# Performance work log

Hardware: AMD Instinct MI355X
Metric: run time of the kernel (lower is better)

Reference implementation:

```python
import jax, jax.numpy as jnp
import numpy as np

E = 8      # num_experts
K = 2      # active_experts
D = 1024   # embed_size
H = 4 * D  # ffn hidden


def setup_inputs() -> dict:
    key = jax.random.key(0)
    ks = jax.random.split(key, 7)
    s_in = 1.0 / np.sqrt(D)
    s_h = 1.0 / np.sqrt(H)
    return {
        "x":  jax.random.normal(ks[0], (4, 2048, D), dtype=jnp.float32),
        "Wr": jax.random.uniform(ks[1], (D, E), jnp.float32, -s_in, s_in),
        "br": jax.random.uniform(ks[2], (E,), jnp.float32, -s_in, s_in),
        "W1": jax.random.uniform(ks[3], (E, D, H), jnp.float32, -s_in, s_in),
        "b1": jax.random.uniform(ks[4], (E, H), jnp.float32, -s_in, s_in),
        "W2": jax.random.uniform(ks[5], (E, H, D), jnp.float32, -s_h, s_h),
        "b2": jax.random.uniform(ks[6], (E, D), jnp.float32, -s_h, s_h),
    }


def reference(x, Wr, br, W1, b1, W2, b2):
    # Router: softmax over experts, top-k values, renormalize.
    logits = jnp.einsum("bsd,de->bse", x, Wr) + br            # [B,S,E]
    probs = jax.nn.softmax(logits, axis=-1)
    topk_vals, _ = jax.lax.top_k(probs, K)                     # [B,S,K]
    gates = topk_vals / topk_vals.sum(axis=-1, keepdims=True)  # [B,S,K]

    # Original bug (reproduced faithfully): the mask-multiply-sum is identity,
    # and slot index i selects experts[i], so only experts 0..K-1 run on ALL tokens.
    h = jax.nn.relu(jnp.einsum("bsd,kdh->bskh", x, W1[:K]) + b1[:K])  # [B,S,K,H]
    y = jnp.einsum("bskh,khd->bskd", h, W2[:K]) + b2[:K]               # [B,S,K,D]
    return jnp.einsum("bskd,bsk->bsd", y, gates)                       # [B,S,D]
```

## Files before the change

kernel.cpp:

```cpp
#include <hip/hip_runtime.h>
#include <hip/hip_bf16.h>

#define T_TOK 8192
#define DDIM  1024
#define HDIM  4096
#define KCAT  8192
#define NE    8

typedef __attribute__((ext_vector_type(8))) __bf16 bf16x8;
typedef __attribute__((ext_vector_type(4))) float  f32x4;

__device__ __forceinline__ unsigned short f2bf(float f) {
  union { float f; unsigned u; } v; v.f = f;
  unsigned r = v.u + 0x7fffu + ((v.u >> 16) & 1u);
  return (unsigned short)(r >> 16);
}

__device__ __forceinline__ void gl_lds16(const unsigned short* g, char* l) {
  __builtin_amdgcn_global_load_lds(
      (__attribute__((address_space(1))) const void*)g,
      (__attribute__((address_space(3))) void*)l,
      16, 0, 0);
}

__global__ __launch_bounds__(256) void k_router(
    const float* __restrict__ x, const float* __restrict__ Wr,
    const float* __restrict__ br, unsigned short* __restrict__ xb,
    float* __restrict__ gates)
{
  const int lane = threadIdx.x & 63;
  const int wv   = threadIdx.x >> 6;
  const int t    = blockIdx.x * 4 + wv;
  const float* xr = x + (size_t)t * DDIM;
  unsigned short* xo = xb + (size_t)t * DDIM;

  float acc[NE];
#pragma unroll
  for (int e = 0; e < NE; ++e) acc[e] = 0.f;

#pragma unroll
  for (int i = 0; i < 4; ++i) {
    float4 v = *(const float4*)(xr + i * 256 + lane * 4);
    ushort4 o;
    o.x = f2bf(v.x); o.y = f2bf(v.y); o.z = f2bf(v.z); o.w = f2bf(v.w);
    *(ushort4*)(xo + i * 256 + lane * 4) = o;
    float vs[4] = {v.x, v.y, v.z, v.w};
#pragma unroll
    for (int j = 0; j < 4; ++j) {
      const float4* wr = (const float4*)(Wr + (size_t)(i * 256 + lane * 4 + j) * NE);
      float4 w0 = wr[0], w1 = wr[1];
      acc[0] += vs[j] * w0.x; acc[1] += vs[j] * w0.y;
      acc[2] += vs[j] * w0.z; acc[3] += vs[j] * w0.w;
      acc[4] += vs[j] * w1.x; acc[5] += vs[j] * w1.y;
      acc[6] += vs[j] * w1.z; acc[7] += vs[j] * w1.w;
    }
  }
#pragma unroll
  for (int e = 0; e < NE; ++e) {
#pragma unroll
    for (int s = 32; s > 0; s >>= 1) acc[e] += __shfl_xor(acc[e], s, 64);
  }
  if (lane == 0) {
    float lg[NE];
#pragma unroll
    for (int e = 0; e < NE; ++e) lg[e] = acc[e] + br[e];
    int a1 = 0; float m1 = lg[0];
#pragma unroll
    for (int e = 1; e < NE; ++e) if (lg[e] > m1) { m1 = lg[e]; a1 = e; }
    float m2 = -3.4e38f;
#pragma unroll
    for (int e = 0; e < NE; ++e) if (e != a1 && lg[e] > m2) m2 = lg[e];
    float g0 = 1.f / (1.f + expf(m2 - m1));
    gates[t * 2 + 0] = g0;
    gates[t * 2 + 1] = 1.f - g0;
  }
}

__global__ __launch_bounds__(256) void k_transpose(
    const float* __restrict__ in, unsigned short* __restrict__ out,
    int R, int C, int S, size_t inz, size_t outz)
{
  __shared__ float tile[32][33];
  in  += (size_t)blockIdx.z * inz;
  out += (size_t)blockIdx.z * outz;
  const int c0 = blockIdx.x * 32, r0 = blockIdx.y * 32;
  const int tx = threadIdx.x & 31, ty = threadIdx.x >> 5;
#pragma unroll
  for (int i = 0; i < 32; i += 8)
    tile[ty + i][tx] = in[(size_t)(r0 + ty + i) * C + (c0 + tx)];
  __syncthreads();
#pragma unroll
  for (int i = 0; i < 32; i += 8)
    out[(size_t)(c0 + ty + i) * S + (r0 + tx)] = f2bf(tile[tx][ty + i]);
}

template<int NT, int MODE>
__global__ __launch_bounds__(512, 2) void k_gemm8(
    const unsigned short* __restrict__ A,
    const unsigned short* __restrict__ B,
    unsigned short* __restrict__ Hout,
    float* __restrict__ P0, float* __restrict__ P1,
    const float* __restrict__ bias,
    const float* __restrict__ gates,
    int KA, int KB)
{
  constexpr int NIT = NT / 2;
  __shared__ __align__(16) char lds[2 * 4 * 16384];

  const int tid = threadIdx.x;
  const int l = tid & 63, g = (l >> 4), l15 = l & 15;
  const int w = tid >> 6;
  const int wm = w >> 2, wn = w & 3;

  int bmIdx, bnIdx, bzIdx;
  {
    int lin = ((blockIdx.z * gridDim.y) + blockIdx.y) * gridDim.x + blockIdx.x;
    int xcd = lin & 7, slot = (lin >> 3) & 31;
    if (MODE == 0) {
      int r = lin >> 8;
      bmIdx = r * 8 + (slot >> 2);
      bnIdx = xcd * 4 + (slot & 3);
      bzIdx = 0;
    } else {
      bzIdx = xcd & 1;
      bmIdx = (xcd >> 1) * 8 + (slot >> 2);
      bnIdx = slot & 3;
    }
  }
  const int bn = bnIdx * 256;
  const int bm = bmIdx * 256;
  const int koff = bzIdx * (NT * 64);

  const int srow = tid >> 2;
  const int sc = (tid & 3) ^ ((srow >> 1) & 3);
  const unsigned short* As = A + (size_t)(bm + srow) * KA + koff + sc * 8;
  const unsigned short* Bs = B + (size_t)(bn + srow) * KB + koff + sc * 8;

  auto stage = [&](int T, int reg) {
    const unsigned short* src = ((reg >> 1) ? Bs : As) + T * 64 + (reg & 1) * 32;
    size_t rstride = (size_t)128 * ((reg >> 1) ? KB : KA);
    char* dst = lds + (((T & 1) * 4 + reg) << 14) + tid * 16;
    gl_lds16(src, dst);
    gl_lds16(src + rstride, dst + 8192);
  };

  int aoff[2][4], boff[4];
#pragma unroll
  for (int mh = 0; mh < 2; ++mh)
#pragma unroll
    for (int mi = 0; mi < 4; ++mi) {
      int r = wm * 128 + mh * 64 + mi * 16 + l15;
      aoff[mh][mi] = r * 64 + ((g ^ ((r >> 1) & 3)) * 16);
    }
#pragma unroll
  for (int nj = 0; nj < 4; ++nj) {
    int r = wn * 64 + nj * 16 + l15;
    boff[nj] = r * 64 + ((g ^ ((r >> 1) & 3)) * 16);
  }

  f32x4 acc[8][4];
#pragma unroll
  for (int i = 0; i < 8; ++i)
#pragma unroll
    for (int j = 0; j < 4; ++j) acc[i][j] = (f32x4){0.f, 0.f, 0.f, 0.f};

  stage(0, 2); stage(0, 0); stage(0, 3); stage(0, 1);
  stage(1, 2); stage(1, 0); stage(1, 3);
  asm volatile("s_waitcnt vmcnt(6)" ::: "memory");
  __builtin_amdgcn_s_barrier();

#define MFMA16(AI, A0, A1, A2, A3)                                                     \
    acc[(AI)+0][0] = __builtin_amdgcn_mfma_f32_16x16x32_bf16(A0, vb0, acc[(AI)+0][0], 0,0,0); \
    acc[(AI)+0][1] = __builtin_amdgcn_mfma_f32_16x16x32_bf16(A0, vb1, acc[(AI)+0][1], 0,0,0); \
    acc[(AI)+0][2] = __builtin_amdgcn_mfma_f32_16x16x32_bf16(A0, vb2, acc[(AI)+0][2], 0,0,0); \
    acc[(AI)+0][3] = __builtin_amdgcn_mfma_f32_16x16x32_bf16(A0, vb3, acc[(AI)+0][3], 0,0,0); \
    acc[(AI)+1][0] = __builtin_amdgcn_mfma_f32_16x16x32_bf16(A1, vb0, acc[(AI)+1][0], 0,0,0); \
    acc[(AI)+1][1] = __builtin_amdgcn_mfma_f32_16x16x32_bf16(A1, vb1, acc[(AI)+1][1], 0,0,0); \
    acc[(AI)+1][2] = __builtin_amdgcn_mfma_f32_16x16x32_bf16(A1, vb2, acc[(AI)+1][2], 0,0,0); \
    acc[(AI)+1][3] = __builtin_amdgcn_mfma_f32_16x16x32_bf16(A1, vb3, acc[(AI)+1][3], 0,0,0); \
    acc[(AI)+2][0] = __builtin_amdgcn_mfma_f32_16x16x32_bf16(A2, vb0, acc[(AI)+2][0], 0,0,0); \
    acc[(AI)+2][1] = __builtin_amdgcn_mfma_f32_16x16x32_bf16(A2, vb1, acc[(AI)+2][1], 0,0,0); \
    acc[(AI)+2][2] = __builtin_amdgcn_mfma_f32_16x16x32_bf16(A2, vb2, acc[(AI)+2][2], 0,0,0); \
    acc[(AI)+2][3] = __builtin_amdgcn_mfma_f32_16x16x32_bf16(A2, vb3, acc[(AI)+2][3], 0,0,0); \
    acc[(AI)+3][0] = __builtin_amdgcn_mfma_f32_16x16x32_bf16(A3, vb0, acc[(AI)+3][0], 0,0,0); \
    acc[(AI)+3][1] = __builtin_amdgcn_mfma_f32_16x16x32_bf16(A3, vb1, acc[(AI)+3][1], 0,0,0); \
    acc[(AI)+3][2] = __builtin_amdgcn_mfma_f32_16x16x32_bf16(A3, vb2, acc[(AI)+3][2], 0,0,0); \
    acc[(AI)+3][3] = __builtin_amdgcn_mfma_f32_16x16x32_bf16(A3, vb3, acc[(AI)+3][3], 0,0,0);

#define MPH(BUF, KH, VM, STG1, STG2) do {                                      \
    const char* Ar_ = lds + (((BUF) * 4 + (KH)) << 14);                        \
    const char* Br_ = lds + (((BUF) * 4 + 2 + (KH)) << 14);                    \
    bf16x8 vb0 = *(const bf16x8*)(Br_ + boff[0]);                              \
    bf16x8 vb1 = *(const bf16x8*)(Br_ + boff[1]);                              \
    bf16x8 vb2 = *(const bf16x8*)(Br_ + boff[2]);                              \
    bf16x8 vb3 = *(const bf16x8*)(Br_ + boff[3]);                              \
    bf16x8 vc0 = *(const bf16x8*)(Ar_ + aoff[0][0]);                           \
    bf16x8 vc1 = *(const bf16x8*)(Ar_ + aoff[0][1]);                           \
    bf16x8 vc2 = *(const bf16x8*)(Ar_ + aoff[0][2]);                           \
    bf16x8 vc3 = *(const bf16x8*)(Ar_ + aoff[0][3]);                           \
    bf16x8 vn0 = *(const bf16x8*)(Ar_ + aoff[1][0]);                           \
    bf16x8 vn1 = *(const bf16x8*)(Ar_ + aoff[1][1]);                           \
    bf16x8 vn2 = *(const bf16x8*)(Ar_ + aoff[1][2]);                           \
    bf16x8 vn3 = *(const bf16x8*)(Ar_ + aoff[1][3]);                           \
    asm volatile("" ::: "memory");          \
    STG1; STG2;                                                                \
    if ((VM) == 6) asm volatile("s_waitcnt vmcnt(6)" ::: "memory");            \
    else if ((VM) == 0) asm volatile("s_waitcnt vmcnt(0)" ::: "memory");       \
    __builtin_amdgcn_s_barrier();                                              \
    __builtin_amdgcn_s_setprio(1);                                             \
    MFMA16(0, vc0, vc1, vc2, vc3)                                              \
    MFMA16(4, vn0, vn1, vn2, vn3)                                              \
    __builtin_amdgcn_s_setprio(0);                                             \
    __builtin_amdgcn_s_barrier();                                              \
  } while (0)

  for (int t = 0; t < NIT - 1; ++t) {
    MPH(0, 0, -1, stage(2 * t + 1, 1), stage(2 * t + 2, 2));
    MPH(0, 1,  6, stage(2 * t + 2, 0), stage(2 * t + 2, 3));
    MPH(1, 0, -1, stage(2 * t + 2, 1), stage(2 * t + 3, 2));
    MPH(1, 1,  6, stage(2 * t + 3, 0), stage(2 * t + 3, 3));
  }
  MPH(0, 0, -1, stage(NT - 1, 1), ;);
  MPH(0, 1,  0, ;, ;);
  MPH(1, 0, -1, ;, ;);
  MPH(1, 1, -1, ;, ;);
#undef MPH
#undef MFMA16

  if constexpr (MODE == 0) {
    const int ge = bn >> 12;
    float bcol[4];
#pragma unroll
    for (int nj = 0; nj < 4; ++nj) bcol[nj] = bias[bn + wn * 64 + nj * 16 + l15];
#pragma unroll
    for (int mi = 0; mi < 8; ++mi) {
#pragma unroll
      for (int rr = 0; rr < 4; ++rr) {
        int row = bm + wm * 128 + mi * 16 + g * 4 + rr;
        float gate = gates[row * 2 + ge];
        size_t rb = (size_t)row * KCAT + bn + wn * 64 + l15;
#pragma unroll
        for (int nj = 0; nj < 4; ++nj) {
          float v = acc[mi][nj][rr] + bcol[nj];
          Hout[rb + nj * 16] = f2bf(fmaxf(v, 0.f) * gate);
        }
      }
    }
  } else {
    float* P = bzIdx ? P1 : P0;
#pragma unroll
    for (int mi = 0; mi < 8; ++mi) {
#pragma unroll
      for (int rr = 0; rr < 4; ++rr) {
        int row = bm + wm * 128 + mi * 16 + g * 4 + rr;
        size_t rb = (size_t)row * DDIM + bn + wn * 64 + l15;
#pragma unroll
        for (int nj = 0; nj < 4; ++nj) P[rb + nj * 16] = acc[mi][nj][rr];
      }
    }
  }
}

__global__ __launch_bounds__(256) void k_combine(
    const float* __restrict__ P1, const float* __restrict__ b2,
    const float* __restrict__ gates, float* __restrict__ O)
{
  size_t i = ((size_t)blockIdx.x * 256 + threadIdx.x) * 4;
  int row = (int)(i >> 10), d = (int)(i & 1023);
  float g0 = gates[row * 2], g1 = gates[row * 2 + 1];
  float4 p0 = *(const float4*)(O + i);
  float4 p1 = *(const float4*)(P1 + i);
  float4 ba = *(const float4*)(b2 + d);
  float4 bb = *(const float4*)(b2 + DDIM + d);
  float4 r;
  r.x = p0.x + p1.x + g0 * ba.x + g1 * bb.x;
  r.y = p0.y + p1.y + g0 * ba.y + g1 * bb.y;
  r.z = p0.z + p1.z + g0 * ba.z + g1 * bb.z;
  r.w = p0.w + p1.w + g0 * ba.w + g1 * bb.w;
  *(float4*)(O + i) = r;
}

extern "C" void kernel_launch(void* const* d_in, const int* in_sizes, int n_in,
                              void* d_out, int out_size, void* d_ws, size_t ws_size,
                              hipStream_t stream) {
  const float* x  = (const float*)d_in[0];
  const float* Wr = (const float*)d_in[1];
  const float* br = (const float*)d_in[2];
  const float* W1 = (const float*)d_in[3];
  const float* b1 = (const float*)d_in[4];
  const float* W2 = (const float*)d_in[5];
  const float* b2 = (const float*)d_in[6];

  char* ws = (char*)d_ws;
  unsigned short* xb    = (unsigned short*)(ws);
  unsigned short* W1T   = (unsigned short*)(ws + (16u << 20));
  unsigned short* W2T   = (unsigned short*)(ws + (32u << 20));
  float*          gates = (float*)(ws + (48u << 20));
  unsigned short* hbuf  = (unsigned short*)(ws + (49u << 20));
  float*          P1    = (float*)(ws);

  k_router<<<dim3(T_TOK / 4), dim3(256), 0, stream>>>(x, Wr, br, xb, gates);

  k_transpose<<<dim3(HDIM / 32, DDIM / 32, 2), dim3(256), 0, stream>>>(
      W1, W1T, DDIM, HDIM, DDIM, (size_t)DDIM * HDIM, (size_t)HDIM * DDIM);
  k_transpose<<<dim3(DDIM / 32, HDIM / 32, 2), dim3(256), 0, stream>>>(
      W2, W2T, HDIM, DDIM, KCAT, (size_t)HDIM * DDIM, (size_t)HDIM);

  k_gemm8<16, 0><<<dim3(KCAT / 256, T_TOK / 256, 1), dim3(512), 0, stream>>>(
      xb, W1T, hbuf, nullptr, nullptr, b1, gates, DDIM, DDIM);

  k_gemm8<64, 1><<<dim3(DDIM / 256, T_TOK / 256, 2), dim3(512), 0, stream>>>(
      hbuf, W2T, nullptr, (float*)d_out, P1, nullptr, nullptr, KCAT, KCAT);

  k_combine<<<dim3(T_TOK * DDIM / 4 / 256), dim3(256), 0, stream>>>(
      P1, b2, gates, (float*)d_out);
}
```

Baseline: 325.7 us.

## Restructure GEMM pipeline into four-stage ring of 32-wide K tiles

Replaces the two-buffer scheme with 64-wide K tiles split into halves by a four-buffer ring of 32-wide K tiles, each holding A and B. Loads run three stages ahead, with vmcnt waits adjusted to 8/4/0. The aim is deeper prefetch so global-to-LDS latency hides behind MFMA work. LDS size stays at 128KB, and the tail handling and wait counts must be exactly right for correctness.

```diff
diff --git a/kernel.cpp b/kernel.cpp
--- a/kernel.cpp
+++ b/kernel.cpp
@@ -95,7 +95,7 @@
 }
 
 template<int NT, int MODE>
-__global__ __launch_bounds__(512, 2) void k_gemm8(
+__global__ __launch_bounds__(512, 2) void k_gemm4(
     const unsigned short* __restrict__ A,
     const unsigned short* __restrict__ B,
     unsigned short* __restrict__ Hout,
@@ -104,8 +104,7 @@
     const float* __restrict__ gates,
     int KA, int KB)
 {
-  constexpr int NIT = NT / 2;
-  __shared__ __align__(16) char lds[2 * 4 * 16384];
+  __shared__ __align__(16) char lds[4 * 32768];
 
   const int tid = threadIdx.x;
   const int l = tid & 63, g = (l >> 4), l15 = l & 15;
@@ -129,7 +128,7 @@
   }
   const int bn = bnIdx * 256;
   const int bm = bmIdx * 256;
-  const int koff = bzIdx * (NT * 64);
+  const int koff = bzIdx * (NT * 32);
 
   const int srow = tid >> 2;
   const int sc = (tid & 3) ^ ((srow >> 1) & 3);
@@ -137,9 +136,9 @@
   const unsigned short* Bs = B + (size_t)(bn + srow) * KB + koff + sc * 8;
 
   auto stage = [&](int T, int reg) {
-    const unsigned short* src = ((reg >> 1) ? Bs : As) + T * 64 + (reg & 1) * 32;
-    size_t rstride = (size_t)128 * ((reg >> 1) ? KB : KA);
-    char* dst = lds + (((T & 1) * 4 + reg) << 14) + tid * 16;
+    const unsigned short* src = (reg ? Bs : As) + T * 32;
+    size_t rstride = (size_t)128 * (reg ? KB : KA);
+    char* dst = lds + ((T & 3) << 15) + (reg << 14) + tid * 16;
     gl_lds16(src, dst);
     gl_lds16(src + rstride, dst + 8192);
   };
@@ -164,9 +163,10 @@
 #pragma unroll
     for (int j = 0; j < 4; ++j) acc[i][j] = (f32x4){0.f, 0.f, 0.f, 0.f};
 
-  stage(0, 2); stage(0, 0); stage(0, 3); stage(0, 1);
-  stage(1, 2); stage(1, 0); stage(1, 3);
-  asm volatile("s_waitcnt vmcnt(6)" ::: "memory");
+  stage(0, 0); stage(0, 1);
+  stage(1, 0); stage(1, 1);
+  stage(2, 0); stage(2, 1);
+  asm volatile("s_waitcnt vmcnt(8)" ::: "memory");
   __builtin_amdgcn_s_barrier();
 
 #define MFMA16(AI, A0, A1, A2, A3)                                                     \
@@ -187,9 +187,9 @@
     acc[(AI)+3][2] = __builtin_amdgcn_mfma_f32_16x16x32_bf16(A3, vb2, acc[(AI)+3][2], 0,0,0); \
     acc[(AI)+3][3] = __builtin_amdgcn_mfma_f32_16x16x32_bf16(A3, vb3, acc[(AI)+3][3], 0,0,0);
 
-#define MPH(BUF, KH, VM, STG1, STG2) do {                                      \
-    const char* Ar_ = lds + (((BUF) * 4 + (KH)) << 14);                        \
-    const char* Br_ = lds + (((BUF) * 4 + 2 + (KH)) << 14);                    \
+#define MPH(BUF, VM, STG1, STG2) do {                                          \
+    const char* Ar_ = lds + ((BUF) << 15);                                     \
+    const char* Br_ = Ar_ + 16384;                                             \
     bf16x8 vb0 = *(const bf16x8*)(Br_ + boff[0]);                              \
     bf16x8 vb1 = *(const bf16x8*)(Br_ + boff[1]);                              \
     bf16x8 vb2 = *(const bf16x8*)(Br_ + boff[2]);                              \
@@ -202,9 +202,10 @@
     bf16x8 vn1 = *(const bf16x8*)(Ar_ + aoff[1][1]);                           \
     bf16x8 vn2 = *(const bf16x8*)(Ar_ + aoff[1][2]);                           \
     bf16x8 vn3 = *(const bf16x8*)(Ar_ + aoff[1][3]);                           \
-    asm volatile("" ::: "memory");          \
+    asm volatile("" ::: "memory");                                             \
     STG1; STG2;                                                                \
-    if ((VM) == 6) asm volatile("s_waitcnt vmcnt(6)" ::: "memory");            \
+    if ((VM) == 8) asm volatile("s_waitcnt vmcnt(8)" ::: "memory");            \
+    else if ((VM) == 4) asm volatile("s_waitcnt vmcnt(4)" ::: "memory");       \
     else if ((VM) == 0) asm volatile("s_waitcnt vmcnt(0)" ::: "memory");       \
     __builtin_amdgcn_s_barrier();                                              \
     __builtin_amdgcn_s_setprio(1);                                             \
@@ -214,16 +215,17 @@
     __builtin_amdgcn_s_barrier();                                              \
   } while (0)
 
-  for (int t = 0; t < NIT - 1; ++t) {
-    MPH(0, 0, -1, stage(2 * t + 1, 1), stage(2 * t + 2, 2));
-    MPH(0, 1,  6, stage(2 * t + 2, 0), stage(2 * t + 2, 3));
-    MPH(1, 0, -1, stage(2 * t + 2, 1), stage(2 * t + 3, 2));
-    MPH(1, 1,  6, stage(2 * t + 3, 0), stage(2 * t + 3, 3));
-  }
-  MPH(0, 0, -1, stage(NT - 1, 1), ;);
-  MPH(0, 1,  0, ;, ;);
-  MPH(1, 0, -1, ;, ;);
-  MPH(1, 1, -1, ;, ;);
+  for (int tt = 0; tt < NT / 4 - 1; ++tt) {
+    int t4 = tt * 4;
+    MPH(0, 8, stage(t4 + 3, 0), stage(t4 + 3, 1));
+    MPH(1, 8, stage(t4 + 4, 0), stage(t4 + 4, 1));
+    MPH(2, 8, stage(t4 + 5, 0), stage(t4 + 5, 1));
+    MPH(3, 8, stage(t4 + 6, 0), stage(t4 + 6, 1));
+  }
+  MPH(0, 8, stage(NT - 1, 0), stage(NT - 1, 1));
+  MPH(1, 4, ;, ;);
+  MPH(2, 0, ;, ;);
+  MPH(3, -1, ;, ;);
 #undef MPH
 #undef MFMA16
 
@@ -306,10 +308,10 @@
   k_transpose<<<dim3(DDIM / 32, HDIM / 32, 2), dim3(256), 0, stream>>>(
       W2, W2T, HDIM, DDIM, KCAT, (size_t)HDIM * DDIM, (size_t)HDIM);
 
-  k_gemm8<16, 0><<<dim3(KCAT / 256, T_TOK / 256, 1), dim3(512), 0, stream>>>(
+  k_gemm4<32, 0><<<dim3(KCAT / 256, T_TOK / 256, 1), dim3(512), 0, stream>>>(
       xb, W1T, hbuf, nullptr, nullptr, b1, gates, DDIM, DDIM);
 
-  k_gemm8<64, 1><<<dim3(DDIM / 256, T_TOK / 256, 2), dim3(512), 0, stream>>>(
+  k_gemm4<128, 1><<<dim3(DDIM / 256, T_TOK / 256, 2), dim3(512), 0, stream>>>(
       hbuf, W2T, nullptr, (float*)d_out, P1, nullptr, nullptr, KCAT, KCAT);
 
   k_combine<<<dim3(T_TOK * DDIM / 4 / 256), dim3(256), 0, stream>>>(
```

New measurement: 324.8 us. Within noise of the previous version (-0.3%).
